# Kernel optimization log

Measured on AMD Instinct MI355X. Metric: run time of the kernel, lower is better.

Reference implementation:

```python
import jax, jax.numpy as jnp
import numpy as np

B, S, V, E, U, L = 32, 256, 32000, 512, 512, 2

def setup_inputs() -> dict:
    key = jax.random.key(0)
    ks = jax.random.split(key, 16)
    def p(k, shape, scale):
        return jax.random.normal(k, shape, dtype=jnp.float32) * scale
    inp = {
        "x": jax.random.randint(ks[0], (B, S), 0, V),
        "state": jnp.zeros((2 * L, B, U), jnp.float32),
        "emb_table": p(ks[1], (V, E), 0.05),
    }
    names = ["fk0", "frk0", "fb0", "fk1", "frk1", "fb1",
             "bk0", "brk0", "bb0", "bk1", "brk1", "bb1"]
    i = 2
    for n in names:
        if n.endswith("b0") or n.endswith("b1"):
            inp[n] = jnp.zeros((2, 3 * U), jnp.float32)
        else:
            inp[n] = p(ks[i], (512, 3 * U), 1.0 / np.sqrt(512))
        i += 1
    return inp

def gru_step(h, xt, k, rk, b):
    # TF2 GRUCell, reset_after=True
    mx = xt @ k + b[0]
    mi = h @ rk + b[1]
    xz, xr, xh = jnp.split(mx, 3, axis=-1)
    iz, ir, ih = jnp.split(mi, 3, axis=-1)
    z = jax.nn.sigmoid(xz + iz)
    r = jax.nn.sigmoid(xr + ir)
    hh = jnp.tanh(xh + r * ih)
    return z * h + (1.0 - z) * hh

def run_rnn(emb_s, mask_s, h0s, params):
    # emb_s: [S,B,E], mask_s: [S,B], h0s: tuple of L x [B,U]
    def step(carry, inp):
        hs, prev = carry
        xt, mt = inp
        m = mt[:, None]
        new_hs = []
        a = xt
        for h, (k, rk, b) in zip(hs, params):
            hn = gru_step(h, a, k, rk, b)
            hn = jnp.where(m, hn, h)  # masked steps carry state
            new_hs.append(hn)
            a = hn
        out = jnp.where(m, a, prev)  # masked steps repeat prev output
        return (tuple(new_hs), out), out
    init = (tuple(h0s), jnp.zeros((emb_s.shape[1], U), emb_s.dtype))
    (hs_f, _), ys = jax.lax.scan(step, init, (emb_s, mask_s))
    return ys, hs_f

def reference(x, state, emb_table,
              fk0, frk0, fb0, fk1, frk1, fb1,
              bk0, brk0, bb0, bk1, brk1, bb1):
    emb = emb_table[x]                      # [B,S,E]
    mask = (x != 0)                         # mask_zero=True
    emb_s = jnp.swapaxes(emb, 0, 1)         # [S,B,E]
    mask_s = jnp.swapaxes(mask, 0, 1)       # [S,B]
    fw_params = [(fk0, frk0, fb0), (fk1, frk1, fb1)]
    bw_params = [(bk0, brk0, bb0), (bk1, brk1, bb1)]
    ys_f, hs_f = run_rnn(emb_s, mask_s, (state[0], state[1]), fw_params)
    ys_b, hs_b = run_rnn(emb_s[::-1], mask_s[::-1], (state[2], state[3]), bw_params)
    ys_b = ys_b[::-1]
    y = jnp.concatenate([ys_f, ys_b], axis=-1)   # [S,B,2U]
    y = jnp.swapaxes(y, 0, 1)                    # [B,S,2U]
    states = jnp.stack(list(hs_f) + list(hs_b), axis=0)  # [2L,B,U]
    return y, states
```

## Files before the change

### kernel.cpp

```cpp
#include <hip/hip_runtime.h>
#include <hip/hip_bf16.h>

#define S_LEN 256
#define NB 32
#define UDIM 512
#define WGS 32
#define FPAD 32

typedef __attribute__((ext_vector_type(8))) short bf16x8;
typedef __attribute__((ext_vector_type(4))) float f32x4;
typedef __attribute__((ext_vector_type(4))) unsigned u32x4;

struct WPtrs { const float* p[8]; };
struct BPtrs { const float* p[4]; };

__device__ __forceinline__ unsigned short f2bf(float f) {
  union { float f; unsigned u; } v; v.f = f;
  unsigned r = v.u + 0x7fffu + ((v.u >> 16) & 1u);
  return (unsigned short)(r >> 16);
}

__device__ __forceinline__ int ld_flag(const int* p) {
  int v;
  asm volatile("global_load_dword %0, %1, off sc0 sc1\n\ts_waitcnt vmcnt(0)"
               : "=&v"(v) : "v"(p) : "memory");
  return v;
}
__device__ __forceinline__ void st_u32c(unsigned* p, unsigned v) {
  asm volatile("global_store_dword %0, %1, off sc0 sc1" :: "v"(p), "v"(v) : "memory");
}
__device__ __forceinline__ void st_flag(int* p, int v) {
  asm volatile("global_store_dword %0, %1, off sc0 sc1" :: "v"(p), "v"(v) : "memory");
}

__device__ __forceinline__ bool ld_hist16(const short* p0, const short* p1,
                                          bf16x8* afr0, bf16x8* afr1) {
  u32x4 q0,q1,q2,q3,q4,q5,q6,q7,q8,q9,q10,q11,q12,q13,q14,q15;
  asm volatile(
    "global_load_dwordx4 %0, %16, off sc0 sc1\n\t"
    "global_load_dwordx4 %1, %16, off offset:64 sc0 sc1\n\t"
    "global_load_dwordx4 %2, %16, off offset:128 sc0 sc1\n\t"
    "global_load_dwordx4 %3, %16, off offset:192 sc0 sc1\n\t"
    "global_load_dwordx4 %4, %16, off offset:256 sc0 sc1\n\t"
    "global_load_dwordx4 %5, %16, off offset:320 sc0 sc1\n\t"
    "global_load_dwordx4 %6, %16, off offset:384 sc0 sc1\n\t"
    "global_load_dwordx4 %7, %16, off offset:448 sc0 sc1\n\t"
    "global_load_dwordx4 %8, %17, off sc0 sc1\n\t"
    "global_load_dwordx4 %9, %17, off offset:64 sc0 sc1\n\t"
    "global_load_dwordx4 %10, %17, off offset:128 sc0 sc1\n\t"
    "global_load_dwordx4 %11, %17, off offset:192 sc0 sc1\n\t"
    "global_load_dwordx4 %12, %17, off offset:256 sc0 sc1\n\t"
    "global_load_dwordx4 %13, %17, off offset:320 sc0 sc1\n\t"
    "global_load_dwordx4 %14, %17, off offset:384 sc0 sc1\n\t"
    "global_load_dwordx4 %15, %17, off offset:448 sc0 sc1\n\t"
    "s_waitcnt vmcnt(0)"
    : "=&v"(q0),"=&v"(q1),"=&v"(q2),"=&v"(q3),"=&v"(q4),"=&v"(q5),"=&v"(q6),"=&v"(q7),
      "=&v"(q8),"=&v"(q9),"=&v"(q10),"=&v"(q11),"=&v"(q12),"=&v"(q13),"=&v"(q14),"=&v"(q15)
    : "v"(p0), "v"(p1)
    : "memory");
  const unsigned S = 0xFFFFFFFFu;
  bool bad = false;
#define CK(q) bad |= (q[0]==S)|(q[1]==S)|(q[2]==S)|(q[3]==S)
  CK(q0);CK(q1);CK(q2);CK(q3);CK(q4);CK(q5);CK(q6);CK(q7);
  CK(q8);CK(q9);CK(q10);CK(q11);CK(q12);CK(q13);CK(q14);CK(q15);
#undef CK
  union U { u32x4 u; bf16x8 b; } cv;
  cv.u=q0;  afr0[0]=cv.b; cv.u=q1;  afr0[1]=cv.b; cv.u=q2;  afr0[2]=cv.b; cv.u=q3;  afr0[3]=cv.b;
  cv.u=q4;  afr0[4]=cv.b; cv.u=q5;  afr0[5]=cv.b; cv.u=q6;  afr0[6]=cv.b; cv.u=q7;  afr0[7]=cv.b;
  cv.u=q8;  afr1[0]=cv.b; cv.u=q9;  afr1[1]=cv.b; cv.u=q10; afr1[2]=cv.b; cv.u=q11; afr1[3]=cv.b;
  cv.u=q12; afr1[4]=cv.b; cv.u=q13; afr1[5]=cv.b; cv.u=q14; afr1[6]=cv.b; cv.u=q15; afr1[7]=cv.b;
  return !bad;
}

__global__ void k_embed(const int* __restrict__ x, const float* __restrict__ tab,
                        unsigned short* __restrict__ emb, int* __restrict__ mask) {
  int t = blockIdx.x, b = blockIdx.y;
  int tok = x[b * S_LEN + t];
  if (threadIdx.x == 0) mask[t * NB + b] = (tok != 0);
  const float4* src = (const float4*)(tab + (size_t)tok * UDIM);
  ushort4* dst = (ushort4*)(emb + ((size_t)t * NB + b) * UDIM);
  int i = threadIdx.x;
  float4 v = src[i];
  ushort4 o;
  o.x = f2bf(v.x); o.y = f2bf(v.y); o.z = f2bf(v.z); o.w = f2bf(v.w);
  dst[i] = o;
}

__global__ void k_wprep(WPtrs wp, unsigned short* __restrict__ wsW) {
  int bid = blockIdx.x;
  int kt = bid & 31; bid >>= 5;
  int g  = bid % 3;  bid /= 3;
  int wg = bid & 31; bid >>= 5;
  int slab = bid;
  const float* src = wp.p[slab];
  int tid = threadIdx.x;
  int r = tid >> 4, cc = tid & 15;
  __shared__ float ldsT[16][17];
  ldsT[cc][r] = src[(size_t)(kt * 16 + r) * 1536 + g * 512 + wg * 16 + cc];
  __syncthreads();
  size_t off = ((size_t)slab * WGS + wg) * (48 * 512) + (size_t)(g * 16 + r) * 512 + kt * 16 + cc;
  wsW[off] = f2bf(ldsT[r][cc]);
}

__global__ __launch_bounds__(256, 1) void k_rnn(
    const unsigned short* __restrict__ wsW, const unsigned short* __restrict__ emb,
    unsigned short* __restrict__ hist, const int* __restrict__ mask,
    int* __restrict__ flags, const float* __restrict__ state,
    BPtrs bp, float* __restrict__ out) {
  __shared__ short sW[2 * 48 * 512];
  __shared__ float sAcc[2][2][2][32][48];
  __shared__ float sBias[2][48];
  __shared__ unsigned char sMask[S_LEN][NB];

  int tid = threadIdx.x;
  int bid = blockIdx.x;
  int xcd = bid & 7;
  int c = xcd >> 1;
  int w = ((bid >> 3) << 1) | (xcd & 1);
  int layer = c & 1;
  bool back = (c >= 2);
  int lane = tid & 63;
  int wave = tid >> 6;
  int mat = wave & 1;
  int kh = wave >> 1;

  int cb = tid >> 3;
  int cj = (tid & 7) << 1;
  float hreg0, hreg1, preg0 = 0.f, preg1 = 0.f;

  {
    const size_t slabSz = 48 * 512;
    for (int ch = tid; ch < 2 * 48 * 64; ch += 256) {
      int m = ch / (48 * 64);
      int rem = ch % (48 * 64);
      int nl = rem >> 6;
      int k16 = rem & 63;
      const unsigned short* sp =
          wsW + ((size_t)((c * 2 + m) * WGS) + w) * slabSz + (size_t)nl * 512 + k16 * 8;
      bf16x8 val = *(const bf16x8*)sp;
      int byte = m * 49152 + nl * 1024 + ((k16 * 16) ^ ((nl & 7) << 4));
      *(bf16x8*)((char*)sW + byte) = val;
    }
    const float* bptr = bp.p[c];
    for (int i = tid; i < 96; i += 256) {
      int m = i / 48, nl = i % 48;
      int col = (nl / 16) * 512 + w * 16 + (nl & 15);
      sBias[m][nl] = bptr[m * 1536 + col];
    }
    for (int i = tid; i < S_LEN * NB; i += 256)
      sMask[i >> 5][i & 31] = (unsigned char)(mask[i] != 0);
    int col = w * 16 + cj;
    hreg0 = state[((size_t)c * NB + cb) * UDIM + col];
    hreg1 = state[((size_t)c * NB + cb) * UDIM + col + 1];
    unsigned pk = (unsigned)f2bf(hreg0) | ((unsigned)f2bf(hreg1) << 16);
    st_u32c((unsigned*)(hist + (((size_t)c * 257) * NB + cb) * UDIM + col), pk);
  }
  __syncthreads();
  if (tid == 0) st_flag(&flags[((c * 257) * 32 + w) * FPAD], 1);

  int r15 = lane & 15, quad = lane >> 4;
  int abase = r15 * UDIM + kh * 256 + quad * 8;
  int matbase = mat * 49152;

  for (int t = 0; t < S_LEN; ++t) {
    int par = t & 1;
    int treal = back ? (S_LEN - 1 - t) : t;
    const unsigned short* arow;
    const int* fl = nullptr;
    int ownIdx = -1;
    if (mat == 0) {
      if (layer == 0) {
        arow = emb + (size_t)treal * NB * UDIM;
      } else {
        arow = hist + ((size_t)(c - 1) * 257 + (t + 1)) * NB * UDIM;
        fl = flags + ((c - 1) * 257 + (t + 1)) * 32 * FPAD;
      }
    } else {
      arow = hist + ((size_t)c * 257 + t) * NB * UDIM;
      fl = flags + (c * 257 + t) * 32 * FPAD;
      ownIdx = w;
    }

    const short* a16 = (const short*)arow;
    const short* p0 = a16 + abase;
    const short* p1 = p0 + 16 * UDIM;

    bf16x8 afr0[8], afr1[8];
    if (fl) {
      const int* fp = fl + (lane & 31) * FPAD;
      bool sub = ((lane & 31) == ownIdx);
      int v = sub ? 1 : ld_flag(fp);
      while (!__all(v != 0)) v = sub ? 1 : ld_flag(fp);
      bool ok = ld_hist16(p0, p1, afr0, afr1);
      while (!__all(ok)) ok = ld_hist16(p0, p1, afr0, afr1);
    } else {
#pragma unroll
      for (int kc = 0; kc < 8; ++kc) {
        afr0[kc] = *(const bf16x8*)(p0 + kc * 32);
        afr1[kc] = *(const bf16x8*)(p1 + kc * 32);
      }
    }

    f32x4 acc[2][3];
#pragma unroll
    for (int a = 0; a < 2; a++)
#pragma unroll
      for (int g = 0; g < 3; g++) acc[a][g] = (f32x4){0.f, 0.f, 0.f, 0.f};
#pragma unroll
    for (int kc = 0; kc < 8; ++kc) {
#pragma unroll
      for (int g = 0; g < 3; ++g) {
        int nl = g * 16 + r15;
        int koff = kh * 512 + kc * 64 + quad * 16;
        int byte = matbase + nl * 1024 + (koff ^ ((nl & 7) << 4));
        bf16x8 bw = *(const bf16x8*)((const char*)sW + byte);
        acc[0][g] = __builtin_amdgcn_mfma_f32_16x16x32_bf16(afr0[kc], bw, acc[0][g], 0, 0, 0);
        acc[1][g] = __builtin_amdgcn_mfma_f32_16x16x32_bf16(afr1[kc], bw, acc[1][g], 0, 0, 0);
      }
    }
#pragma unroll
    for (int mt = 0; mt < 2; ++mt)
#pragma unroll
      for (int g = 0; g < 3; ++g)
#pragma unroll
        for (int rr = 0; rr < 4; ++rr)
          sAcc[par][kh][mat][mt * 16 + quad * 4 + rr][g * 16 + r15] = acc[mt][g][rr];
    __syncthreads();

    float hn0, hn1;
    bool mk;
    {
      int b = cb, j0 = cj;
      mk = sMask[treal][b] != 0;
#pragma unroll
      for (int u = 0; u < 2; ++u) {
        int j = j0 + u;
        float az = sAcc[par][0][0][b][j]      + sAcc[par][1][0][b][j]      + sBias[0][j];
        float ar = sAcc[par][0][0][b][16 + j] + sAcc[par][1][0][b][16 + j] + sBias[0][16 + j];
        float ah = sAcc[par][0][0][b][32 + j] + sAcc[par][1][0][b][32 + j] + sBias[0][32 + j];
        float iz = sAcc[par][0][1][b][j]      + sAcc[par][1][1][b][j]      + sBias[1][j];
        float ir = sAcc[par][0][1][b][16 + j] + sAcc[par][1][1][b][16 + j] + sBias[1][16 + j];
        float ih = sAcc[par][0][1][b][32 + j] + sAcc[par][1][1][b][32 + j] + sBias[1][32 + j];
        float z = 1.f / (1.f + __expf(-(az + iz)));
        float r = 1.f / (1.f + __expf(-(ar + ir)));
        float pre = ah + r * ih;
        pre = fminf(fmaxf(pre, -30.f), 30.f);
        float e2 = __expf(2.f * pre);
        float hh = (e2 - 1.f) / (e2 + 1.f);
        float hold = (u == 0) ? hreg0 : hreg1;
        float hv = z * hold + (1.f - z) * hh;
        hv = mk ? hv : hold;
        if (u == 0) hn0 = hv; else hn1 = hv;
      }
      hreg0 = hn0; hreg1 = hn1;
      unsigned pk = (unsigned)f2bf(hn0) | ((unsigned)f2bf(hn1) << 16);
      st_u32c((unsigned*)(hist + (((size_t)c * 257 + (t + 1)) * NB + cb) * UDIM + w * 16 + j0), pk);
    }
    __builtin_amdgcn_s_barrier();
    if (tid == 0) st_flag(&flags[((c * 257 + (t + 1)) * 32 + w) * FPAD], 1);

    if (layer == 1) {
      float o0 = mk ? hn0 : preg0;
      float o1 = mk ? hn1 : preg1;
      preg0 = o0; preg1 = o1;
      *(float2*)(out + ((size_t)cb * S_LEN + treal) * 1024 + (back ? 512 : 0) + w * 16 + cj) =
          make_float2(o0, o1);
    }
    if (t == S_LEN - 1) {
      *(float2*)(out + (size_t)NB * S_LEN * 1024 + ((size_t)c * NB + cb) * UDIM + w * 16 + cj) =
          make_float2(hn0, hn1);
    }
  }
}

extern "C" void kernel_launch(void* const* d_in, const int* in_sizes, int n_in,
                              void* d_out, int out_size, void* d_ws, size_t ws_size,
                              hipStream_t stream) {
  const int* x = (const int*)d_in[0];
  const float* state = (const float*)d_in[1];
  const float* tab = (const float*)d_in[2];
  WPtrs wp;
  wp.p[0] = (const float*)d_in[3];
  wp.p[1] = (const float*)d_in[4];
  wp.p[2] = (const float*)d_in[6];
  wp.p[3] = (const float*)d_in[7];
  wp.p[4] = (const float*)d_in[9];
  wp.p[5] = (const float*)d_in[10];
  wp.p[6] = (const float*)d_in[12];
  wp.p[7] = (const float*)d_in[13];
  BPtrs bp;
  bp.p[0] = (const float*)d_in[5];
  bp.p[1] = (const float*)d_in[8];
  bp.p[2] = (const float*)d_in[11];
  bp.p[3] = (const float*)d_in[14];
  float* out = (float*)d_out;

  char* ws = (char*)d_ws;
  size_t off = 0;
  unsigned short* wsW = (unsigned short*)(ws + off); off += (size_t)8 * 32 * 48 * 512 * 2;
  unsigned short* embp = (unsigned short*)(ws + off); off += (size_t)S_LEN * NB * UDIM * 2;
  unsigned short* hist = (unsigned short*)(ws + off);
  size_t histBytes = (size_t)4 * 257 * NB * UDIM * 2;  off += histBytes;
  int* maskp = (int*)(ws + off); off += (size_t)S_LEN * NB * 4;
  int* flags = (int*)(ws + off);
  size_t flagBytes = (size_t)4 * 257 * 32 * FPAD * 4;  off += flagBytes;

  hipMemsetAsync(hist, 0xFF, histBytes, stream);
  hipMemsetAsync(flags, 0, flagBytes, stream);
  k_embed<<<dim3(S_LEN, NB), 128, 0, stream>>>(x, tab, embp, maskp);
  k_wprep<<<8 * 32 * 3 * 32, 256, 0, stream>>>(wp, wsW);
  k_rnn<<<128, 256, 0, stream>>>(wsW, embp, hist, maskp, flags, state, bp, out);
}
```

Before: 1.123 ms.

## Store hidden-state history in per-workgroup slabs and pack flags contiguously

The hidden-state history buffer changes from row-major [batch, unit] order to per-workgroup 1 KB slabs, so each producer workgroup writes one contiguous region. Consumers load A fragments with new offsets and the interleaving is remapped to match. Flags lose their 32-int padding, so each flag sits in one 128-byte line that a wave can read in a single coalesced load. This aims to cut cross-workgroup polling and history load latency, at the cost of false sharing among flag writers on the same cache line.

```diff
diff --git a/kernel.cpp b/kernel.cpp
--- a/kernel.cpp
+++ b/kernel.cpp
@@ -5,7 +5,6 @@
 #define NB 32
 #define UDIM 512
 #define WGS 32
-#define FPAD 32
 
 typedef __attribute__((ext_vector_type(8))) short bf16x8;
 typedef __attribute__((ext_vector_type(4))) float f32x4;
@@ -13,6 +12,8 @@
 
 struct WPtrs { const float* p[8]; };
 struct BPtrs { const float* p[4]; };
+
+#define SLAB(c, slot) ((((size_t)(c) * 257 + (slot)) * 32) << 10)
 
 __device__ __forceinline__ unsigned short f2bf(float f) {
   union { float f; unsigned u; } v; v.f = f;
@@ -26,37 +27,38 @@
                : "=&v"(v) : "v"(p) : "memory");
   return v;
 }
-__device__ __forceinline__ void st_u32c(unsigned* p, unsigned v) {
+__device__ __forceinline__ void st_u32c(void* p, unsigned v) {
   asm volatile("global_store_dword %0, %1, off sc0 sc1" :: "v"(p), "v"(v) : "memory");
 }
 __device__ __forceinline__ void st_flag(int* p, int v) {
   asm volatile("global_store_dword %0, %1, off sc0 sc1" :: "v"(p), "v"(v) : "memory");
 }
 
-__device__ __forceinline__ bool ld_hist16(const short* p0, const short* p1,
+__device__ __forceinline__ bool ld_slab16(const char* b0, const char* b1,
+                                          const char* b2, const char* b3,
                                           bf16x8* afr0, bf16x8* afr1) {
   u32x4 q0,q1,q2,q3,q4,q5,q6,q7,q8,q9,q10,q11,q12,q13,q14,q15;
   asm volatile(
     "global_load_dwordx4 %0, %16, off sc0 sc1\n\t"
-    "global_load_dwordx4 %1, %16, off offset:64 sc0 sc1\n\t"
-    "global_load_dwordx4 %2, %16, off offset:128 sc0 sc1\n\t"
-    "global_load_dwordx4 %3, %16, off offset:192 sc0 sc1\n\t"
-    "global_load_dwordx4 %4, %16, off offset:256 sc0 sc1\n\t"
-    "global_load_dwordx4 %5, %16, off offset:320 sc0 sc1\n\t"
-    "global_load_dwordx4 %6, %16, off offset:384 sc0 sc1\n\t"
-    "global_load_dwordx4 %7, %16, off offset:448 sc0 sc1\n\t"
-    "global_load_dwordx4 %8, %17, off sc0 sc1\n\t"
-    "global_load_dwordx4 %9, %17, off offset:64 sc0 sc1\n\t"
-    "global_load_dwordx4 %10, %17, off offset:128 sc0 sc1\n\t"
-    "global_load_dwordx4 %11, %17, off offset:192 sc0 sc1\n\t"
-    "global_load_dwordx4 %12, %17, off offset:256 sc0 sc1\n\t"
-    "global_load_dwordx4 %13, %17, off offset:320 sc0 sc1\n\t"
-    "global_load_dwordx4 %14, %17, off offset:384 sc0 sc1\n\t"
-    "global_load_dwordx4 %15, %17, off offset:448 sc0 sc1\n\t"
+    "global_load_dwordx4 %1, %16, off offset:512 sc0 sc1\n\t"
+    "global_load_dwordx4 %2, %16, off offset:2048 sc0 sc1\n\t"
+    "global_load_dwordx4 %3, %16, off offset:2560 sc0 sc1\n\t"
+    "global_load_dwordx4 %4, %17, off sc0 sc1\n\t"
+    "global_load_dwordx4 %5, %17, off offset:512 sc0 sc1\n\t"
+    "global_load_dwordx4 %6, %17, off offset:2048 sc0 sc1\n\t"
+    "global_load_dwordx4 %7, %17, off offset:2560 sc0 sc1\n\t"
+    "global_load_dwordx4 %8, %18, off sc0 sc1\n\t"
+    "global_load_dwordx4 %9, %18, off offset:512 sc0 sc1\n\t"
+    "global_load_dwordx4 %10, %18, off offset:2048 sc0 sc1\n\t"
+    "global_load_dwordx4 %11, %18, off offset:2560 sc0 sc1\n\t"
+    "global_load_dwordx4 %12, %19, off sc0 sc1\n\t"
+    "global_load_dwordx4 %13, %19, off offset:512 sc0 sc1\n\t"
+    "global_load_dwordx4 %14, %19, off offset:2048 sc0 sc1\n\t"
+    "global_load_dwordx4 %15, %19, off offset:2560 sc0 sc1\n\t"
     "s_waitcnt vmcnt(0)"
     : "=&v"(q0),"=&v"(q1),"=&v"(q2),"=&v"(q3),"=&v"(q4),"=&v"(q5),"=&v"(q6),"=&v"(q7),
       "=&v"(q8),"=&v"(q9),"=&v"(q10),"=&v"(q11),"=&v"(q12),"=&v"(q13),"=&v"(q14),"=&v"(q15)
-    : "v"(p0), "v"(p1)
+    : "v"(b0), "v"(b1), "v"(b2), "v"(b3)
     : "memory");
   const unsigned S = 0xFFFFFFFFu;
   bool bad = false;
@@ -65,10 +67,10 @@
   CK(q8);CK(q9);CK(q10);CK(q11);CK(q12);CK(q13);CK(q14);CK(q15);
 #undef CK
   union U { u32x4 u; bf16x8 b; } cv;
-  cv.u=q0;  afr0[0]=cv.b; cv.u=q1;  afr0[1]=cv.b; cv.u=q2;  afr0[2]=cv.b; cv.u=q3;  afr0[3]=cv.b;
-  cv.u=q4;  afr0[4]=cv.b; cv.u=q5;  afr0[5]=cv.b; cv.u=q6;  afr0[6]=cv.b; cv.u=q7;  afr0[7]=cv.b;
-  cv.u=q8;  afr1[0]=cv.b; cv.u=q9;  afr1[1]=cv.b; cv.u=q10; afr1[2]=cv.b; cv.u=q11; afr1[3]=cv.b;
-  cv.u=q12; afr1[4]=cv.b; cv.u=q13; afr1[5]=cv.b; cv.u=q14; afr1[6]=cv.b; cv.u=q15; afr1[7]=cv.b;
+  cv.u=q0;  afr0[0]=cv.b; cv.u=q1;  afr1[0]=cv.b; cv.u=q2;  afr0[1]=cv.b; cv.u=q3;  afr1[1]=cv.b;
+  cv.u=q4;  afr0[2]=cv.b; cv.u=q5;  afr1[2]=cv.b; cv.u=q6;  afr0[3]=cv.b; cv.u=q7;  afr1[3]=cv.b;
+  cv.u=q8;  afr0[4]=cv.b; cv.u=q9;  afr1[4]=cv.b; cv.u=q10; afr0[5]=cv.b; cv.u=q11; afr1[5]=cv.b;
+  cv.u=q12; afr0[6]=cv.b; cv.u=q13; afr1[6]=cv.b; cv.u=q14; afr0[7]=cv.b; cv.u=q15; afr1[7]=cv.b;
   return !bad;
 }
 
@@ -128,6 +130,8 @@
   int cj = (tid & 7) << 1;
   float hreg0, hreg1, preg0 = 0.f, preg1 = 0.f;
 
+  char* histc = (char*)hist;
+
   {
     const size_t slabSz = 48 * 512;
     for (int ch = tid; ch < 2 * 48 * 64; ch += 256) {
@@ -153,52 +157,48 @@
     hreg0 = state[((size_t)c * NB + cb) * UDIM + col];
     hreg1 = state[((size_t)c * NB + cb) * UDIM + col + 1];
     unsigned pk = (unsigned)f2bf(hreg0) | ((unsigned)f2bf(hreg1) << 16);
-    st_u32c((unsigned*)(hist + (((size_t)c * 257) * NB + cb) * UDIM + col), pk);
+    st_u32c(histc + SLAB(c, 0) + ((size_t)w << 10) + cb * 32 + cj * 2, pk);
   }
   __syncthreads();
-  if (tid == 0) st_flag(&flags[((c * 257) * 32 + w) * FPAD], 1);
+  if (tid == 0) st_flag(&flags[(c * 257) * 32 + w], 1);
 
   int r15 = lane & 15, quad = lane >> 4;
+  int lbase = ((kh * 16 + (quad >> 1)) << 10) + ((quad & 1) << 4) + r15 * 32;
   int abase = r15 * UDIM + kh * 256 + quad * 8;
   int matbase = mat * 49152;
 
   for (int t = 0; t < S_LEN; ++t) {
     int par = t & 1;
     int treal = back ? (S_LEN - 1 - t) : t;
-    const unsigned short* arow;
-    const int* fl = nullptr;
-    int ownIdx = -1;
-    if (mat == 0) {
-      if (layer == 0) {
-        arow = emb + (size_t)treal * NB * UDIM;
-      } else {
-        arow = hist + ((size_t)(c - 1) * 257 + (t + 1)) * NB * UDIM;
-        fl = flags + ((c - 1) * 257 + (t + 1)) * 32 * FPAD;
+
+    bf16x8 afr0[8], afr1[8];
+    if (mat == 0 && layer == 0) {
+      const short* a16 = (const short*)(emb + (size_t)treal * NB * UDIM);
+#pragma unroll
+      for (int kc = 0; kc < 8; ++kc) {
+        afr0[kc] = *(const bf16x8*)(a16 + abase + kc * 32);
+        afr1[kc] = *(const bf16x8*)(a16 + abase + 16 * UDIM + kc * 32);
       }
     } else {
-      arow = hist + ((size_t)c * 257 + t) * NB * UDIM;
-      fl = flags + (c * 257 + t) * 32 * FPAD;
-      ownIdx = w;
-    }
-
-    const short* a16 = (const short*)arow;
-    const short* p0 = a16 + abase;
-    const short* p1 = p0 + 16 * UDIM;
-
-    bf16x8 afr0[8], afr1[8];
-    if (fl) {
-      const int* fp = fl + (lane & 31) * FPAD;
+      const int* fl;
+      const char* sb;
+      int ownIdx = -1;
+      if (mat == 0) {
+        sb = histc + SLAB(c - 1, t + 1);
+        fl = flags + ((c - 1) * 257 + (t + 1)) * 32;
+      } else {
+        sb = histc + SLAB(c, t);
+        fl = flags + (c * 257 + t) * 32;
+        ownIdx = w;
+      }
+      const int* fp = fl + (lane & 31);
       bool sub = ((lane & 31) == ownIdx);
       int v = sub ? 1 : ld_flag(fp);
       while (!__all(v != 0)) v = sub ? 1 : ld_flag(fp);
-      bool ok = ld_hist16(p0, p1, afr0, afr1);
-      while (!__all(ok)) ok = ld_hist16(p0, p1, afr0, afr1);
-    } else {
-#pragma unroll
-      for (int kc = 0; kc < 8; ++kc) {
-        afr0[kc] = *(const bf16x8*)(p0 + kc * 32);
-        afr1[kc] = *(const bf16x8*)(p1 + kc * 32);
-      }
+      const char* b0 = sb + lbase;
+      bool ok = ld_slab16(b0, b0 + 4096, b0 + 8192, b0 + 12288, afr0, afr1);
+      while (!__all(ok))
+        ok = ld_slab16(b0, b0 + 4096, b0 + 8192, b0 + 12288, afr0, afr1);
     }
 
     f32x4 acc[2][3];
@@ -254,10 +254,10 @@
       }
       hreg0 = hn0; hreg1 = hn1;
       unsigned pk = (unsigned)f2bf(hn0) | ((unsigned)f2bf(hn1) << 16);
-      st_u32c((unsigned*)(hist + (((size_t)c * 257 + (t + 1)) * NB + cb) * UDIM + w * 16 + j0), pk);
+      st_u32c(histc + SLAB(c, t + 1) + ((size_t)w << 10) + cb * 32 + cj * 2, pk);
     }
     __builtin_amdgcn_s_barrier();
-    if (tid == 0) st_flag(&flags[((c * 257 + (t + 1)) * 32 + w) * FPAD], 1);
+    if (tid == 0) st_flag(&flags[(c * 257 + (t + 1)) * 32 + w], 1);
 
     if (layer == 1) {
       float o0 = mk ? hn0 : preg0;
@@ -300,10 +300,10 @@
   unsigned short* wsW = (unsigned short*)(ws + off); off += (size_t)8 * 32 * 48 * 512 * 2;
   unsigned short* embp = (unsigned short*)(ws + off); off += (size_t)S_LEN * NB * UDIM * 2;
   unsigned short* hist = (unsigned short*)(ws + off);
-  size_t histBytes = (size_t)4 * 257 * NB * UDIM * 2;  off += histBytes;
+  size_t histBytes = (size_t)4 * 257 * 32 * 1024;      off += histBytes;
   int* maskp = (int*)(ws + off); off += (size_t)S_LEN * NB * 4;
   int* flags = (int*)(ws + off);
-  size_t flagBytes = (size_t)4 * 257 * 32 * FPAD * 4;  off += flagBytes;
+  size_t flagBytes = (size_t)4 * 257 * 32 * 4;         off += flagBytes;
 
   hipMemsetAsync(hist, 0xFF, histBytes, stream);
   hipMemsetAsync(flags, 0, flagBytes, stream);
```

Result: faster. 994.6 us (-11.4%).
